# Optimization experiments

Hardware: AMD Instinct MI355X
Metric: run time of the kernel (lower is better)

## Reference

```python
import jax, jax.numpy as jnp
import numpy as np

E = 128            # emb_size
N_TEXT = 40000     # text entities
N_NONTEXT = 10000  # non-text entities
N = N_TEXT + N_NONTEXT
N_EDGES = 300000
N_REL = 500
I = 3              # num_intents
ROUNDS = 2
RROUNDS = 2
PE = 2             # topic one-hot width
PRED_IN = 5 * E + 2 * PE + 2 * PE * (ROUNDS + RROUNDS)  # 5*128+4+16 = 660


def setup_inputs() -> dict:
    key = jax.random.key(0)
    ks = jax.random.split(key, 12)
    return {
        "h_id_tensor": jax.random.randint(ks[0], (N_EDGES,), 0, N, dtype=jnp.int64 if jax.config.jax_enable_x64 else jnp.int32).astype(jnp.int32),
        "r_id_tensor": jax.random.randint(ks[1], (N_EDGES,), 0, N_REL).astype(jnp.int32),
        "t_id_tensor": jax.random.randint(ks[2], (N_EDGES,), 0, N).astype(jnp.int32),
        "q_emb": jax.random.normal(ks[3], (1, E), dtype=jnp.float32),
        "entity_embs": jax.random.normal(ks[4], (N_TEXT, E), dtype=jnp.float32),
        "num_non_text_entities": N_NONTEXT,
        "relation_embs": jax.random.normal(ks[5], (N_REL, E), dtype=jnp.float32),
        "topic_entity_one_hot": jax.random.uniform(ks[6], (N, PE), dtype=jnp.float32),
        # learned params
        "non_text_entity_emb": jax.random.normal(ks[7], (1, E), dtype=jnp.float32),
        "intent_embs": jax.random.normal(ks[8], (I, E), dtype=jnp.float32),
        "W1": jax.random.normal(ks[9], (PRED_IN, E), dtype=jnp.float32) * 0.02,
        "b1": jnp.zeros((E,), dtype=jnp.float32),
        "W2": jax.random.normal(ks[10], (E, 1), dtype=jnp.float32) * 0.02,
        "b2": jnp.zeros((1,), dtype=jnp.float32),
    }


def _peconv(x, src, dst, n, inv_cnt):
    # mean aggregation: gather x at src, scatter-mean into dst
    s = jax.ops.segment_sum(x[src], dst, num_segments=n)
    return s * inv_cnt


def reference(h_id_tensor, r_id_tensor, t_id_tensor, q_emb, entity_embs,
              num_non_text_entities, relation_embs, topic_entity_one_hot,
              non_text_entity_emb, intent_embs, W1, b1, W2, b2):
    n = topic_entity_one_hot.shape[0]
    h_e0 = jnp.concatenate(
        [entity_embs, jnp.broadcast_to(non_text_entity_emb, (num_non_text_entities, E))], axis=0)  # [N,E]

    ones = jnp.ones((h_id_tensor.shape[0], 1), jnp.float32)
    cnt_fwd = jax.ops.segment_sum(ones, t_id_tensor, num_segments=n)  # in-degree via (h->t)
    cnt_rev = jax.ops.segment_sum(ones, h_id_tensor, num_segments=n)
    inv_fwd = 1.0 / jnp.maximum(cnt_fwd, 1.0)
    inv_rev = 1.0 / jnp.maximum(cnt_rev, 1.0)

    h_e_list = [h_e0, topic_entity_one_hot]
    h_pe = topic_entity_one_hot
    for _ in range(ROUNDS):
        h_pe = _peconv(h_pe, h_id_tensor, t_id_tensor, n, inv_fwd)
        h_e_list.append(h_pe)
    h_pe = topic_entity_one_hot
    for _ in range(RROUNDS):
        h_pe = _peconv(h_pe, t_id_tensor, h_id_tensor, n, inv_rev)
        h_e_list.append(h_pe)
    h_e = jnp.concatenate(h_e_list, axis=1)  # [N, E + 2 + 2*4]

    h_r = relation_embs[r_id_tensor]         # [T, E]
    h_head = h_e[h_id_tensor]                # [T, E+10]
    h_tail = h_e[t_id_tensor]                # [T, E+10]
    T = h_r.shape[0]
    h_q = jnp.broadcast_to(q_emb, (T, E))

    logits = []
    for i in range(intent_embs.shape[0]):
        iv = jnp.broadcast_to(intent_embs[i][None, :], (T, E))
        h_triple = jnp.concatenate([iv, h_q, h_head, h_r, h_tail], axis=1)  # [T, PRED_IN]
        h = jnp.maximum(h_triple @ W1 + b1, 0.0)
        logits.append(h @ W2 + b2)
    return jnp.concatenate(logits, axis=1)  # [T, I]
```

## Files before the change

### kernel.cpp

```cpp
#include <hip/hip_runtime.h>

#define E 128
#define OFF_Q 128
#define OFF_HEAD 256
#define OFF_REL 394
#define OFF_TAIL 522
#define KTOT 138
#define KP 160
#define AST 168
#define RNGC 2048
#define NCHK 8
#define CAP 16384

typedef __attribute__((ext_vector_type(8))) short short8;
typedef __attribute__((ext_vector_type(4))) float f32x4;

__device__ __forceinline__ unsigned short f2bf(float f) {
    unsigned u = __float_as_uint(f);
    return (unsigned short)((u + 0x7fffu + ((u >> 16) & 1u)) >> 16);
}
__device__ __forceinline__ unsigned bpack(float lo, float hi) {
    return (unsigned)f2bf(lo) | ((unsigned)f2bf(hi) << 16);
}
__device__ __forceinline__ float blo(unsigned u) { return __uint_as_float(u << 16); }
__device__ __forceinline__ float bhi(unsigned u) { return __uint_as_float(u & 0xffff0000u); }

__global__ __launch_bounds__(256) void bucket_prep_kernel(
        const int* __restrict__ h_id, const int* __restrict__ t_id,
        const float* __restrict__ rel, const float* __restrict__ intent,
        const float* __restrict__ q, const float* __restrict__ W1,
        const float* __restrict__ b1,
        unsigned* __restrict__ curs, unsigned* __restrict__ pairs_f,
        unsigned* __restrict__ pairs_r,
        unsigned short* __restrict__ rel_bf, float* __restrict__ bias3,
        unsigned short* __restrict__ W1T,
        int T, int bucketBlocks, int relBlocks, int biasBlocks, int NREL) {
    int tid = threadIdx.x;
    int bid = blockIdx.x;

    if (bid < bucketBlocks) {
        __shared__ unsigned hf[32], hr[32], basef[32], baser[32];
        if (tid < 32) { hf[tid] = 0; hr[tid] = 0; }
        __syncthreads();
        int e0 = (bid * 256 + tid) * 4;
        int hh[4], tt[4];
        int cnt = 0;
        if (e0 < T) {
            if (e0 + 3 < T) {
                int4 h4 = *(const int4*)&h_id[e0];
                int4 t4 = *(const int4*)&t_id[e0];
                hh[0] = h4.x; hh[1] = h4.y; hh[2] = h4.z; hh[3] = h4.w;
                tt[0] = t4.x; tt[1] = t4.y; tt[2] = t4.z; tt[3] = t4.w;
                cnt = 4;
            } else {
                for (int j = 0; e0 + j < T && j < 4; ++j) {
                    hh[j] = h_id[e0 + j];
                    tt[j] = t_id[e0 + j];
                    ++cnt;
                }
            }
        }
        unsigned bf[4], br[4];
        for (int j = 0; j < cnt; ++j) {
            bf[j] = (unsigned)tt[j] >> 11;
            br[j] = (unsigned)hh[j] >> 11;
            atomicAdd(&hf[bf[j]], 1u);
            atomicAdd(&hr[br[j]], 1u);
        }
        __syncthreads();
        if (tid < 32) {
            basef[tid] = hf[tid] ? atomicAdd(&curs[tid], hf[tid]) : 0u;
            baser[tid] = hr[tid] ? atomicAdd(&curs[32 + tid], hr[tid]) : 0u;
        }
        __syncthreads();
        if (tid < 32) { hf[tid] = 0; hr[tid] = 0; }
        __syncthreads();
        for (int j = 0; j < cnt; ++j) {
            unsigned sf = basef[bf[j]] + atomicAdd(&hf[bf[j]], 1u);
            if (sf < CAP) pairs_f[bf[j] * CAP + sf] =
                (unsigned)hh[j] | (((unsigned)tt[j] & 2047u) << 16);
            unsigned sr = baser[br[j]] + atomicAdd(&hr[br[j]], 1u);
            if (sr < CAP) pairs_r[br[j] * CAP + sr] =
                (unsigned)tt[j] | (((unsigned)hh[j] & 2047u) << 16);
        }
    } else if (bid < bucketBlocks + relBlocks) {
        int idx = (bid - bucketBlocks) * 256 + tid;
        int r = idx >> 7, j = idx & 127;
        if (r < NREL) {
            const float4* xr = (const float4*)(rel + (size_t)r * E);
            float acc = 0.f;
#pragma unroll
            for (int k4 = 0; k4 < 32; ++k4) {
                float4 x = xr[k4];
                int k = OFF_REL + k4 * 4;
                acc = fmaf(x.x, W1[(k + 0) * E + j], acc);
                acc = fmaf(x.y, W1[(k + 1) * E + j], acc);
                acc = fmaf(x.z, W1[(k + 2) * E + j], acc);
                acc = fmaf(x.w, W1[(k + 3) * E + j], acc);
            }
            rel_bf[idx] = f2bf(acc);
        }
    } else if (bid < bucketBlocks + relBlocks + biasBlocks) {
        int widx = (bid - bucketBlocks - relBlocks) * 4 + (tid >> 6);
        int lane = tid & 63;
        if (widx < 384) {
            int i = widx >> 7, j = widx & 127;
            float sum = 0.f;
#pragma unroll
            for (int m = 0; m < 4; ++m) {
                int k = lane + 64 * m;
                float x = (k < 128) ? intent[i * E + k] : q[k - 128];
                sum = fmaf(x, W1[(size_t)k * E + j], sum);
            }
#pragma unroll
            for (int o = 32; o > 0; o >>= 1) sum += __shfl_xor(sum, o, 64);
            if (lane == 0) bias3[i * E + j] = sum + b1[j];
        }
    } else {
        int c = bid - bucketBlocks - relBlocks - biasBlocks;
        if (tid < KP) {
            int cc = (c < 128) ? c : c - 128;
            int base = (c < 128) ? OFF_HEAD : OFF_TAIL;
            float v = (tid < KTOT) ? W1[(size_t)(base + tid) * E + cc] : 0.f;
            W1T[(size_t)c * KP + tid] = f2bf(v);
        }
    }
}

__global__ __launch_bounds__(1024) void scat1_kernel(
        const unsigned* __restrict__ pairs_f, const unsigned* __restrict__ pairs_r,
        const unsigned* __restrict__ curs, const float* __restrict__ topic,
        float* __restrict__ part1) {
    __shared__ float bins[6][RNGC];
    int b = blockIdx.x;
    int ck = blockIdx.y;
    int tid = threadIdx.x;
    for (int i = tid; i < 6 * RNGC; i += 1024) ((float*)bins)[i] = 0.f;
    __syncthreads();
    unsigned cf = min(curs[b], (unsigned)CAP);
    unsigned cr = min(curs[32 + b], (unsigned)CAP);
    const unsigned* pf = pairs_f + (size_t)b * CAP;
    const unsigned* pr = pairs_r + (size_t)b * CAP;
    unsigned lf = (cf + NCHK - 1) / NCHK;
    unsigned lr = (cr + NCHK - 1) / NCHK;
    unsigned f0 = ck * lf, f1e = min(cf, f0 + lf);
    unsigned r0 = ck * lr, r1e = min(cr, r0 + lr);
    for (unsigned i = f0 + tid; i < f1e; i += 1024) {
        unsigned p = pf[i];
        float2 v = *(const float2*)&topic[2 * (size_t)(p & 0xFFFFu)];
        int dl = p >> 16;
        atomicAdd(&bins[0][dl], v.x);
        atomicAdd(&bins[1][dl], v.y);
        atomicAdd(&bins[2][dl], 1.0f);
    }
    for (unsigned i = r0 + tid; i < r1e; i += 1024) {
        unsigned p = pr[i];
        float2 v = *(const float2*)&topic[2 * (size_t)(p & 0xFFFFu)];
        int dl = p >> 16;
        atomicAdd(&bins[3][dl], v.x);
        atomicAdd(&bins[4][dl], v.y);
        atomicAdd(&bins[5][dl], 1.0f);
    }
    __syncthreads();
    float* dst = part1 + ((size_t)(b * NCHK + ck) * 6) * RNGC;
#pragma unroll
    for (int c = 0; c < 6; ++c)
        for (int n = tid; n < RNGC; n += 1024)
            dst[c * RNGC + n] = bins[c][n];
}

__global__ __launch_bounds__(256) void reduce1_kernel(
        const float* __restrict__ part1,
        float* __restrict__ pef1, float* __restrict__ per1,
        float* __restrict__ inv_fwd, float* __restrict__ inv_rev, int N) {
    int n = blockIdx.x * 256 + threadIdx.x;
    if (n >= N) return;
    int b = n >> 11, nl = n & 2047;
    float s[6] = {0.f, 0.f, 0.f, 0.f, 0.f, 0.f};
    const float* base = part1 + (size_t)b * NCHK * 6 * RNGC + nl;
#pragma unroll
    for (int ck = 0; ck < NCHK; ++ck)
#pragma unroll
        for (int c = 0; c < 6; ++c)
            s[c] += base[(ck * 6 + c) * RNGC];
    float invf = 1.0f / fmaxf(s[2], 1.0f);
    float invr = 1.0f / fmaxf(s[5], 1.0f);
    pef1[2 * n] = s[0] * invf;
    pef1[2 * n + 1] = s[1] * invf;
    per1[2 * n] = s[3] * invr;
    per1[2 * n + 1] = s[4] * invr;
    inv_fwd[n] = invf;
    inv_rev[n] = invr;
}

__global__ __launch_bounds__(1024) void scat2_kernel(
        const unsigned* __restrict__ pairs_f, const unsigned* __restrict__ pairs_r,
        const unsigned* __restrict__ curs,
        const float* __restrict__ pef1, const float* __restrict__ per1,
        float* __restrict__ part2) {
    __shared__ float bins[4][RNGC];
    int b = blockIdx.x;
    int ck = blockIdx.y;
    int tid = threadIdx.x;
    for (int i = tid; i < 4 * RNGC; i += 1024) ((float*)bins)[i] = 0.f;
    __syncthreads();
    unsigned cf = min(curs[b], (unsigned)CAP);
    unsigned cr = min(curs[32 + b], (unsigned)CAP);
    const unsigned* pf = pairs_f + (size_t)b * CAP;
    const unsigned* pr = pairs_r + (size_t)b * CAP;
    unsigned lf = (cf + NCHK - 1) / NCHK;
    unsigned lr = (cr + NCHK - 1) / NCHK;
    unsigned f0 = ck * lf, f1e = min(cf, f0 + lf);
    unsigned r0 = ck * lr, r1e = min(cr, r0 + lr);
    for (unsigned i = f0 + tid; i < f1e; i += 1024) {
        unsigned p = pf[i];
        float2 v = *(const float2*)&pef1[2 * (size_t)(p & 0xFFFFu)];
        int dl = p >> 16;
        atomicAdd(&bins[0][dl], v.x);
        atomicAdd(&bins[1][dl], v.y);
    }
    for (unsigned i = r0 + tid; i < r1e; i += 1024) {
        unsigned p = pr[i];
        float2 v = *(const float2*)&per1[2 * (size_t)(p & 0xFFFFu)];
        int dl = p >> 16;
        atomicAdd(&bins[2][dl], v.x);
        atomicAdd(&bins[3][dl], v.y);
    }
    __syncthreads();
    float* dst = part2 + ((size_t)(b * NCHK + ck) * 4) * RNGC;
#pragma unroll
    for (int c = 0; c < 4; ++c)
        for (int n = tid; n < RNGC; n += 1024)
            dst[c * RNGC + n] = bins[c][n];
}

__global__ __launch_bounds__(256) void nodepre_mfma(
        const float* __restrict__ ent, const float* __restrict__ nontext,
        const float* __restrict__ topic,
        const float* __restrict__ pef1, const float* __restrict__ per1,
        const float* __restrict__ part2,
        const float* __restrict__ inv_fwd, const float* __restrict__ inv_rev,
        const unsigned short* __restrict__ W1T,
        unsigned short* __restrict__ head_bf, unsigned short* __restrict__ tail_bf,
        int N, int NTEXT) {
    __shared__ unsigned short As[64 * AST];
    int t = threadIdx.x;
    int lane = t & 63;
    int w = t >> 6;
    int l15 = lane & 15;
    int lg = lane >> 4;
    int n0 = blockIdx.x * 64;

    {
        int row = t >> 2, ch = t & 3;
        int node = n0 + row;
        bool ok = node < N;
        const float* src = (node < NTEXT) ? (ent + (size_t)node * E) : nontext;
        unsigned* dst = (unsigned*)&As[row * AST + ch * 32];
#pragma unroll
        for (int qq = 0; qq < 8; ++qq) {
            float4 v = ok ? *(const float4*)(src + ch * 32 + qq * 4)
                          : make_float4(0.f, 0.f, 0.f, 0.f);
            dst[qq * 2 + 0] = bpack(v.x, v.y);
            dst[qq * 2 + 1] = bpack(v.z, v.w);
        }
    }
    if (t < 64) {
        int node = n0 + t;
        bool ok = node < N;
        unsigned short* dst = &As[t * AST + 128];
        float ex[6];
        if (ok) {
            ex[0] = topic[2 * (size_t)node]; ex[1] = topic[2 * (size_t)node + 1];
            ex[2] = pef1[2 * (size_t)node];  ex[3] = pef1[2 * (size_t)node + 1];
            ex[4] = per1[2 * (size_t)node];  ex[5] = per1[2 * (size_t)node + 1];
        } else {
#pragma unroll
            for (int m = 0; m < 6; ++m) ex[m] = 0.f;
        }
        dst[0] = f2bf(ex[0]); dst[1] = f2bf(ex[1]);
        dst[2] = f2bf(ex[2]); dst[3] = f2bf(ex[3]);
        dst[6] = f2bf(ex[4]); dst[7] = f2bf(ex[5]);
#pragma unroll
        for (int m = 10; m < 32; ++m) dst[m] = 0;
    }
    {
        int nloc = t >> 2;
        int c = t & 3;
        int node = n0 + nloc;
        float val = 0.f;
        if (node < N) {
            int b = node >> 11, nl = node & 2047;
            const float* base = part2 + (size_t)b * NCHK * 4 * RNGC + nl;
            float s = 0.f;
#pragma unroll
            for (int ck = 0; ck < NCHK; ++ck)
                s += base[(ck * 4 + c) * RNGC];
            val = s * ((c < 2) ? inv_fwd[node] : inv_rev[node]);
        }
        int slot = (c < 2) ? (132 + c) : (134 + c);
        As[nloc * AST + (slot - 128) + 128] = f2bf(val);
    }
    __syncthreads();

    f32x4 zero = {0.f, 0.f, 0.f, 0.f};
    f32x4 acc[4][4];
#pragma unroll
    for (int rt = 0; rt < 4; ++rt)
#pragma unroll
        for (int ct = 0; ct < 4; ++ct) acc[rt][ct] = zero;

#pragma unroll
    for (int ks = 0; ks < 5; ++ks) {
        int kb = ks * 32 + lg * 8;
        short8 afrag[4];
#pragma unroll
        for (int rt = 0; rt < 4; ++rt)
            afrag[rt] = *(const short8*)&As[(rt * 16 + l15) * AST + kb];
#pragma unroll
        for (int ct = 0; ct < 4; ++ct) {
            int c = w * 64 + ct * 16 + l15;
            short8 b = *(const short8*)&W1T[(size_t)c * KP + kb];
#pragma unroll
            for (int rt = 0; rt < 4; ++rt)
                acc[rt][ct] = __builtin_amdgcn_mfma_f32_16x16x32_bf16(
                    afrag[rt], b, acc[rt][ct], 0, 0, 0);
        }
    }

#pragma unroll
    for (int rt = 0; rt < 4; ++rt) {
#pragma unroll
        for (int ct = 0; ct < 4; ++ct) {
            int c = w * 64 + ct * 16 + l15;
            unsigned short* base = (c < 128) ? head_bf : tail_bf;
            int cc = (c < 128) ? c : c - 128;
#pragma unroll
            for (int r = 0; r < 4; ++r) {
                int node = n0 + rt * 16 + lg * 4 + r;
                if (node < N) base[(size_t)node * E + cc] = f2bf(acc[rt][ct][r]);
            }
        }
    }
}

__global__ __launch_bounds__(256) void edge_kernel(
        const int* __restrict__ h_id, const int* __restrict__ r_id, const int* __restrict__ t_id,
        const unsigned short* __restrict__ head_bf, const unsigned short* __restrict__ rel_bf,
        const unsigned short* __restrict__ tail_bf, const float* __restrict__ bias3,
        const float* __restrict__ W2, const float* __restrict__ b2,
        float* __restrict__ out, int T) {
    int lane = threadIdx.x & 63;
    int sub = lane >> 4;
    int sl = lane & 15;
    int wid = blockIdx.x * (blockDim.x >> 6) + (threadIdx.x >> 6);
    int nw = gridDim.x * (blockDim.x >> 6);
    int c0 = sl * 8;

    float4 bi0a = *(const float4*)&bias3[c0],         bi0b = *(const float4*)&bias3[c0 + 4];
    float4 bi1a = *(const float4*)&bias3[E + c0],     bi1b = *(const float4*)&bias3[E + c0 + 4];
    float4 bi2a = *(const float4*)&bias3[2 * E + c0], bi2b = *(const float4*)&bias3[2 * E + c0 + 4];
    float4 w2a = *(const float4*)&W2[c0], w2b = *(const float4*)&W2[c0 + 4];
    float b2s = b2[0];

    int qd = lane / 3;
    int md = lane - qd * 3;

    int ne4 = (T + 3) >> 2;
    for (int e4 = wid; e4 < ne4; e4 += nw) {
        int e = e4 * 4 + sub;
        float p0 = 0.f, p1 = 0.f, p2 = 0.f;
        if (e < T) {
            int h = h_id[e], r = r_id[e], tt = t_id[e];
            uint4 hu = *(const uint4*)(head_bf + (size_t)h * E + c0);
            uint4 ru = *(const uint4*)(rel_bf + (size_t)r * E + c0);
            uint4 tu = *(const uint4*)(tail_bf + (size_t)tt * E + c0);
            float sv[8];
            sv[0] = blo(hu.x) + blo(ru.x) + blo(tu.x);
            sv[1] = bhi(hu.x) + bhi(ru.x) + bhi(tu.x);
            sv[2] = blo(hu.y) + blo(ru.y) + blo(tu.y);
            sv[3] = bhi(hu.y) + bhi(ru.y) + bhi(tu.y);
            sv[4] = blo(hu.z) + blo(ru.z) + blo(tu.z);
            sv[5] = bhi(hu.z) + bhi(ru.z) + bhi(tu.z);
            sv[6] = blo(hu.w) + blo(ru.w) + blo(tu.w);
            sv[7] = bhi(hu.w) + bhi(ru.w) + bhi(tu.w);
            float bi0[8] = {bi0a.x, bi0a.y, bi0a.z, bi0a.w, bi0b.x, bi0b.y, bi0b.z, bi0b.w};
            float bi1[8] = {bi1a.x, bi1a.y, bi1a.z, bi1a.w, bi1b.x, bi1b.y, bi1b.z, bi1b.w};
            float bi2[8] = {bi2a.x, bi2a.y, bi2a.z, bi2a.w, bi2b.x, bi2b.y, bi2b.z, bi2b.w};
            float w2v[8] = {w2a.x, w2a.y, w2a.z, w2a.w, w2b.x, w2b.y, w2b.z, w2b.w};
#pragma unroll
            for (int j = 0; j < 8; ++j) {
                p0 = fmaf(fmaxf(sv[j] + bi0[j], 0.f), w2v[j], p0);
                p1 = fmaf(fmaxf(sv[j] + bi1[j], 0.f), w2v[j], p1);
                p2 = fmaf(fmaxf(sv[j] + bi2[j], 0.f), w2v[j], p2);
            }
        }
#pragma unroll
        for (int o = 1; o < 16; o <<= 1) {
            p0 += __shfl_xor(p0, o, 64);
            p1 += __shfl_xor(p1, o, 64);
            p2 += __shfl_xor(p2, o, 64);
        }
        if (e4 * 4 + 3 < T) {
            int srcl = qd * 16;
            float v0 = __shfl(p0, srcl, 64);
            float v1 = __shfl(p1, srcl, 64);
            float v2 = __shfl(p2, srcl, 64);
            if (lane < 12) {
                float v = (md == 0) ? v0 : ((md == 1) ? v1 : v2);
                out[(size_t)e4 * 12 + lane] = v + b2s;
            }
        } else if (e < T && sl < 3) {
            float v = (sl == 0) ? p0 : ((sl == 1) ? p1 : p2);
            out[(size_t)e * 3 + sl] = v + b2s;
        }
    }
}

extern "C" void kernel_launch(void* const* d_in, const int* in_sizes, int n_in,
                              void* d_out, int out_size, void* d_ws, size_t ws_size,
                              hipStream_t stream) {
    const int* h_id = (const int*)d_in[0];
    const int* r_id = (const int*)d_in[1];
    const int* t_id = (const int*)d_in[2];
    const float* q = (const float*)d_in[3];
    const float* ent = (const float*)d_in[4];
    const float* rel = (const float*)d_in[6];
    const float* topic = (const float*)d_in[7];
    const float* nontext = (const float*)d_in[8];
    const float* intent = (const float*)d_in[9];
    const float* W1 = (const float*)d_in[10];
    const float* b1 = (const float*)d_in[11];
    const float* W2 = (const float*)d_in[12];
    const float* b2 = (const float*)d_in[13];

    int T = in_sizes[0];
    int NTEXT = in_sizes[4] / E;
    int N = in_sizes[7] / 2;
    int NREL = in_sizes[6] / E;

    int RC = (N + RNGC - 1) / RNGC;

    unsigned* curs = (unsigned*)d_ws;
    unsigned* pairs_f = curs + 64;
    unsigned* pairs_r = pairs_f + (size_t)32 * CAP;
    float* part1 = (float*)(pairs_r + (size_t)32 * CAP);
    float* inv_fwd = part1 + (size_t)RC * NCHK * 6 * RNGC;
    float* inv_rev = inv_fwd + N;
    float* pef1 = inv_rev + N;
    float* per1 = pef1 + 2 * (size_t)N;
    float* bias3 = per1 + 2 * (size_t)N;
    unsigned short* W1T = (unsigned short*)(bias3 + 3 * E);
    unsigned short* rel_bf = W1T + 256 * KP;
    unsigned short* head_bf = rel_bf + (size_t)NREL * E;
    unsigned short* tail_bf = head_bf + (size_t)N * E;

    const int tb = 256;
    int bucketBlocks = (T + tb * 4 - 1) / (tb * 4);
    int relBlocks = (NREL * E + tb - 1) / tb;
    int biasBlocks = 96;

    hipMemsetAsync(curs, 0, 64 * sizeof(unsigned), stream);

    bucket_prep_kernel<<<bucketBlocks + relBlocks + biasBlocks + 256, tb, 0, stream>>>(
        h_id, t_id, rel, intent, q, W1, b1, curs, pairs_f, pairs_r,
        rel_bf, bias3, W1T, T, bucketBlocks, relBlocks, biasBlocks, NREL);
    scat1_kernel<<<dim3(RC, NCHK), 1024, 0, stream>>>(pairs_f, pairs_r, curs, topic, part1);
    reduce1_kernel<<<(N + tb - 1) / tb, tb, 0, stream>>>(part1, pef1, per1, inv_fwd, inv_rev, N);
    scat2_kernel<<<dim3(RC, NCHK), 1024, 0, stream>>>(pairs_f, pairs_r, curs, pef1, per1, part1);
    nodepre_mfma<<<(N + 63) / 64, tb, 0, stream>>>(ent, nontext, topic, pef1, per1,
                                                   part1, inv_fwd, inv_rev, W1T,
                                                   head_bf, tail_bf, N, NTEXT);
    edge_kernel<<<2048, tb, 0, stream>>>(h_id, r_id, t_id, head_bf, rel_bf, tail_bf,
                                         bias3, W2, b2, (float*)d_out, T);
}
```

Baseline: 111.2 us.

## Fuse bucketing and scatter phases into one cooperative kernel with grid syncs

Merges edge bucketing, first scatter, reduction and second scatter into a single cooperative kernel separated by grid.sync, replacing four launches plus a memset. Weight preprocessing moves into its own kernel. The aim is to cut launch overhead and inter-kernel gaps. The grid is only RC*NCHK = 200 blocks of 1024 threads each holding 48KB of LDS, so bucketing runs with fewer threads and the cooperative launch requires all blocks to be co-resident. The edge kernel also drops its vectorized 12-lane output store in favour of the simpler per-edge store.

```diff
diff --git a/kernel.cpp b/kernel.cpp
--- a/kernel.cpp
+++ b/kernel.cpp
@@ -1,4 +1,7 @@
 #include <hip/hip_runtime.h>
+#include <hip/hip_cooperative_groups.h>
+
+namespace cg = cooperative_groups;
 
 #define E 128
 #define OFF_Q 128
@@ -25,24 +28,26 @@
 __device__ __forceinline__ float blo(unsigned u) { return __uint_as_float(u << 16); }
 __device__ __forceinline__ float bhi(unsigned u) { return __uint_as_float(u & 0xffff0000u); }
 
-__global__ __launch_bounds__(256) void bucket_prep_kernel(
+__global__ __launch_bounds__(1024) void scatter_coop(
         const int* __restrict__ h_id, const int* __restrict__ t_id,
-        const float* __restrict__ rel, const float* __restrict__ intent,
-        const float* __restrict__ q, const float* __restrict__ W1,
-        const float* __restrict__ b1,
+        const float* __restrict__ topic,
         unsigned* __restrict__ curs, unsigned* __restrict__ pairs_f,
-        unsigned* __restrict__ pairs_r,
-        unsigned short* __restrict__ rel_bf, float* __restrict__ bias3,
-        unsigned short* __restrict__ W1T,
-        int T, int bucketBlocks, int relBlocks, int biasBlocks, int NREL) {
+        unsigned* __restrict__ pairs_r, float* __restrict__ part1,
+        float* __restrict__ pef1, float* __restrict__ per1,
+        float* __restrict__ inv_fwd, float* __restrict__ inv_rev,
+        int T, int N) {
+    cg::grid_group grid = cg::this_grid();
+    __shared__ float bins[6][RNGC];
+    __shared__ unsigned hf[32], hr[32], basef[32], baser[32];
     int tid = threadIdx.x;
     int bid = blockIdx.x;
-
-    if (bid < bucketBlocks) {
-        __shared__ unsigned hf[32], hr[32], basef[32], baser[32];
-        if (tid < 32) { hf[tid] = 0; hr[tid] = 0; }
-        __syncthreads();
-        int e0 = (bid * 256 + tid) * 4;
+    int gthreads = gridDim.x * 1024;
+
+    if (bid == 0 && tid < 64) curs[tid] = 0;
+    grid.sync();
+
+    for (int base = 0; base < T; base += gthreads * 4) {
+        int e0 = base + (bid * 1024 + tid) * 4;
         int hh[4], tt[4];
         int cnt = 0;
         if (e0 < T) {
@@ -60,6 +65,8 @@
                 }
             }
         }
+        if (tid < 32) { hf[tid] = 0; hr[tid] = 0; }
+        __syncthreads();
         unsigned bf[4], br[4];
         for (int j = 0; j < cnt; ++j) {
             bf[j] = (unsigned)tt[j] >> 11;
@@ -83,8 +90,115 @@
             if (sr < CAP) pairs_r[br[j] * CAP + sr] =
                 (unsigned)tt[j] | (((unsigned)hh[j] & 2047u) << 16);
         }
-    } else if (bid < bucketBlocks + relBlocks) {
-        int idx = (bid - bucketBlocks) * 256 + tid;
+        __syncthreads();
+    }
+    grid.sync();
+
+    {
+        int b = bid / NCHK;
+        int ck = bid % NCHK;
+        for (int i = tid; i < 6 * RNGC; i += 1024) ((float*)bins)[i] = 0.f;
+        __syncthreads();
+        unsigned cf = min(curs[b], (unsigned)CAP);
+        unsigned cr = min(curs[32 + b], (unsigned)CAP);
+        const unsigned* pf = pairs_f + (size_t)b * CAP;
+        const unsigned* pr = pairs_r + (size_t)b * CAP;
+        unsigned lf = (cf + NCHK - 1) / NCHK;
+        unsigned lr = (cr + NCHK - 1) / NCHK;
+        unsigned f0 = ck * lf, f1e = min(cf, f0 + lf);
+        unsigned r0 = ck * lr, r1e = min(cr, r0 + lr);
+        for (unsigned i = f0 + tid; i < f1e; i += 1024) {
+            unsigned p = pf[i];
+            float2 v = *(const float2*)&topic[2 * (size_t)(p & 0xFFFFu)];
+            int dl = p >> 16;
+            atomicAdd(&bins[0][dl], v.x);
+            atomicAdd(&bins[1][dl], v.y);
+            atomicAdd(&bins[2][dl], 1.0f);
+        }
+        for (unsigned i = r0 + tid; i < r1e; i += 1024) {
+            unsigned p = pr[i];
+            float2 v = *(const float2*)&topic[2 * (size_t)(p & 0xFFFFu)];
+            int dl = p >> 16;
+            atomicAdd(&bins[3][dl], v.x);
+            atomicAdd(&bins[4][dl], v.y);
+            atomicAdd(&bins[5][dl], 1.0f);
+        }
+        __syncthreads();
+        float* dst = part1 + ((size_t)(b * NCHK + ck) * 6) * RNGC;
+#pragma unroll
+        for (int c = 0; c < 6; ++c)
+            for (int n = tid; n < RNGC; n += 1024)
+                dst[c * RNGC + n] = bins[c][n];
+    }
+    grid.sync();
+
+    for (int n = bid * 1024 + tid; n < N; n += gthreads) {
+        int b = n >> 11, nl = n & 2047;
+        float s[6] = {0.f, 0.f, 0.f, 0.f, 0.f, 0.f};
+        const float* pbase = part1 + (size_t)b * NCHK * 6 * RNGC + nl;
+#pragma unroll
+        for (int ck = 0; ck < NCHK; ++ck)
+#pragma unroll
+            for (int c = 0; c < 6; ++c)
+                s[c] += pbase[(ck * 6 + c) * RNGC];
+        float invf = 1.0f / fmaxf(s[2], 1.0f);
+        float invr = 1.0f / fmaxf(s[5], 1.0f);
+        pef1[2 * n] = s[0] * invf;
+        pef1[2 * n + 1] = s[1] * invf;
+        per1[2 * n] = s[3] * invr;
+        per1[2 * n + 1] = s[4] * invr;
+        inv_fwd[n] = invf;
+        inv_rev[n] = invr;
+    }
+    grid.sync();
+
+    {
+        int b = bid / NCHK;
+        int ck = bid % NCHK;
+        for (int i = tid; i < 4 * RNGC; i += 1024) ((float*)bins)[i] = 0.f;
+        __syncthreads();
+        unsigned cf = min(curs[b], (unsigned)CAP);
+        unsigned cr = min(curs[32 + b], (unsigned)CAP);
+        const unsigned* pf = pairs_f + (size_t)b * CAP;
+        const unsigned* pr = pairs_r + (size_t)b * CAP;
+        unsigned lf = (cf + NCHK - 1) / NCHK;
+        unsigned lr = (cr + NCHK - 1) / NCHK;
+        unsigned f0 = ck * lf, f1e = min(cf, f0 + lf);
+        unsigned r0 = ck * lr, r1e = min(cr, r0 + lr);
+        for (unsigned i = f0 + tid; i < f1e; i += 1024) {
+            unsigned p = pf[i];
+            float2 v = *(const float2*)&pef1[2 * (size_t)(p & 0xFFFFu)];
+            int dl = p >> 16;
+            atomicAdd(&bins[0][dl], v.x);
+            atomicAdd(&bins[1][dl], v.y);
+        }
+        for (unsigned i = r0 + tid; i < r1e; i += 1024) {
+            unsigned p = pr[i];
+            float2 v = *(const float2*)&per1[2 * (size_t)(p & 0xFFFFu)];
+            int dl = p >> 16;
+            atomicAdd(&bins[2][dl], v.x);
+            atomicAdd(&bins[3][dl], v.y);
+        }
+        __syncthreads();
+        float* dst = part1 + ((size_t)(b * NCHK + ck) * 4) * RNGC;
+#pragma unroll
+        for (int c = 0; c < 4; ++c)
+            for (int n = tid; n < RNGC; n += 1024)
+                dst[c * RNGC + n] = bins[c][n];
+    }
+}
+
+__global__ __launch_bounds__(256) void prep_kernel(
+        const float* __restrict__ rel, const float* __restrict__ intent,
+        const float* __restrict__ q, const float* __restrict__ W1,
+        const float* __restrict__ b1,
+        unsigned short* __restrict__ rel_bf, float* __restrict__ bias3,
+        unsigned short* __restrict__ W1T,
+        int relBlocks, int biasBlocks, int NREL) {
+    int tid = threadIdx.x;
+    int bid = blockIdx.x;
+    if (bid < relBlocks) {
+        int idx = bid * 256 + tid;
         int r = idx >> 7, j = idx & 127;
         if (r < NREL) {
             const float4* xr = (const float4*)(rel + (size_t)r * E);
@@ -100,8 +214,8 @@
             }
             rel_bf[idx] = f2bf(acc);
         }
-    } else if (bid < bucketBlocks + relBlocks + biasBlocks) {
-        int widx = (bid - bucketBlocks - relBlocks) * 4 + (tid >> 6);
+    } else if (bid < relBlocks + biasBlocks) {
+        int widx = (bid - relBlocks) * 4 + (tid >> 6);
         int lane = tid & 63;
         if (widx < 384) {
             int i = widx >> 7, j = widx & 127;
@@ -117,7 +231,7 @@
             if (lane == 0) bias3[i * E + j] = sum + b1[j];
         }
     } else {
-        int c = bid - bucketBlocks - relBlocks - biasBlocks;
+        int c = bid - relBlocks - biasBlocks;
         if (tid < KP) {
             int cc = (c < 128) ? c : c - 128;
             int base = (c < 128) ? OFF_HEAD : OFF_TAIL;
@@ -125,113 +239,6 @@
             W1T[(size_t)c * KP + tid] = f2bf(v);
         }
     }
-}
-
-__global__ __launch_bounds__(1024) void scat1_kernel(
-        const unsigned* __restrict__ pairs_f, const unsigned* __restrict__ pairs_r,
-        const unsigned* __restrict__ curs, const float* __restrict__ topic,
-        float* __restrict__ part1) {
-    __shared__ float bins[6][RNGC];
-    int b = blockIdx.x;
-    int ck = blockIdx.y;
-    int tid = threadIdx.x;
-    for (int i = tid; i < 6 * RNGC; i += 1024) ((float*)bins)[i] = 0.f;
-    __syncthreads();
-    unsigned cf = min(curs[b], (unsigned)CAP);
-    unsigned cr = min(curs[32 + b], (unsigned)CAP);
-    const unsigned* pf = pairs_f + (size_t)b * CAP;
-    const unsigned* pr = pairs_r + (size_t)b * CAP;
-    unsigned lf = (cf + NCHK - 1) / NCHK;
-    unsigned lr = (cr + NCHK - 1) / NCHK;
-    unsigned f0 = ck * lf, f1e = min(cf, f0 + lf);
-    unsigned r0 = ck * lr, r1e = min(cr, r0 + lr);
-    for (unsigned i = f0 + tid; i < f1e; i += 1024) {
-        unsigned p = pf[i];
-        float2 v = *(const float2*)&topic[2 * (size_t)(p & 0xFFFFu)];
-        int dl = p >> 16;
-        atomicAdd(&bins[0][dl], v.x);
-        atomicAdd(&bins[1][dl], v.y);
-        atomicAdd(&bins[2][dl], 1.0f);
-    }
-    for (unsigned i = r0 + tid; i < r1e; i += 1024) {
-        unsigned p = pr[i];
-        float2 v = *(const float2*)&topic[2 * (size_t)(p & 0xFFFFu)];
-        int dl = p >> 16;
-        atomicAdd(&bins[3][dl], v.x);
-        atomicAdd(&bins[4][dl], v.y);
-        atomicAdd(&bins[5][dl], 1.0f);
-    }
-    __syncthreads();
-    float* dst = part1 + ((size_t)(b * NCHK + ck) * 6) * RNGC;
-#pragma unroll
-    for (int c = 0; c < 6; ++c)
-        for (int n = tid; n < RNGC; n += 1024)
-            dst[c * RNGC + n] = bins[c][n];
-}
-
-__global__ __launch_bounds__(256) void reduce1_kernel(
-        const float* __restrict__ part1,
-        float* __restrict__ pef1, float* __restrict__ per1,
-        float* __restrict__ inv_fwd, float* __restrict__ inv_rev, int N) {
-    int n = blockIdx.x * 256 + threadIdx.x;
-    if (n >= N) return;
-    int b = n >> 11, nl = n & 2047;
-    float s[6] = {0.f, 0.f, 0.f, 0.f, 0.f, 0.f};
-    const float* base = part1 + (size_t)b * NCHK * 6 * RNGC + nl;
-#pragma unroll
-    for (int ck = 0; ck < NCHK; ++ck)
-#pragma unroll
-        for (int c = 0; c < 6; ++c)
-            s[c] += base[(ck * 6 + c) * RNGC];
-    float invf = 1.0f / fmaxf(s[2], 1.0f);
-    float invr = 1.0f / fmaxf(s[5], 1.0f);
-    pef1[2 * n] = s[0] * invf;
-    pef1[2 * n + 1] = s[1] * invf;
-    per1[2 * n] = s[3] * invr;
-    per1[2 * n + 1] = s[4] * invr;
-    inv_fwd[n] = invf;
-    inv_rev[n] = invr;
-}
-
-__global__ __launch_bounds__(1024) void scat2_kernel(
-        const unsigned* __restrict__ pairs_f, const unsigned* __restrict__ pairs_r,
-        const unsigned* __restrict__ curs,
-        const float* __restrict__ pef1, const float* __restrict__ per1,
-        float* __restrict__ part2) {
-    __shared__ float bins[4][RNGC];
-    int b = blockIdx.x;
-    int ck = blockIdx.y;
-    int tid = threadIdx.x;
-    for (int i = tid; i < 4 * RNGC; i += 1024) ((float*)bins)[i] = 0.f;
-    __syncthreads();
-    unsigned cf = min(curs[b], (unsigned)CAP);
-    unsigned cr = min(curs[32 + b], (unsigned)CAP);
-    const unsigned* pf = pairs_f + (size_t)b * CAP;
-    const unsigned* pr = pairs_r + (size_t)b * CAP;
-    unsigned lf = (cf + NCHK - 1) / NCHK;
-    unsigned lr = (cr + NCHK - 1) / NCHK;
-    unsigned f0 = ck * lf, f1e = min(cf, f0 + lf);
-    unsigned r0 = ck * lr, r1e = min(cr, r0 + lr);
-    for (unsigned i = f0 + tid; i < f1e; i += 1024) {
-        unsigned p = pf[i];
-        float2 v = *(const float2*)&pef1[2 * (size_t)(p & 0xFFFFu)];
-        int dl = p >> 16;
-        atomicAdd(&bins[0][dl], v.x);
-        atomicAdd(&bins[1][dl], v.y);
-    }
-    for (unsigned i = r0 + tid; i < r1e; i += 1024) {
-        unsigned p = pr[i];
-        float2 v = *(const float2*)&per1[2 * (size_t)(p & 0xFFFFu)];
-        int dl = p >> 16;
-        atomicAdd(&bins[2][dl], v.x);
-        atomicAdd(&bins[3][dl], v.y);
-    }
-    __syncthreads();
-    float* dst = part2 + ((size_t)(b * NCHK + ck) * 4) * RNGC;
-#pragma unroll
-    for (int c = 0; c < 4; ++c)
-        for (int n = tid; n < RNGC; n += 1024)
-            dst[c * RNGC + n] = bins[c][n];
 }
 
 __global__ __launch_bounds__(256) void nodepre_mfma(
@@ -362,9 +369,6 @@
     float4 bi2a = *(const float4*)&bias3[2 * E + c0], bi2b = *(const float4*)&bias3[2 * E + c0 + 4];
     float4 w2a = *(const float4*)&W2[c0], w2b = *(const float4*)&W2[c0 + 4];
     float b2s = b2[0];
-
-    int qd = lane / 3;
-    int md = lane - qd * 3;
 
     int ne4 = (T + 3) >> 2;
     for (int e4 = wid; e4 < ne4; e4 += nw) {
@@ -401,16 +405,7 @@
             p1 += __shfl_xor(p1, o, 64);
             p2 += __shfl_xor(p2, o, 64);
         }
-        if (e4 * 4 + 3 < T) {
-            int srcl = qd * 16;
-            float v0 = __shfl(p0, srcl, 64);
-            float v1 = __shfl(p1, srcl, 64);
-            float v2 = __shfl(p2, srcl, 64);
-            if (lane < 12) {
-                float v = (md == 0) ? v0 : ((md == 1) ? v1 : v2);
-                out[(size_t)e4 * 12 + lane] = v + b2s;
-            }
-        } else if (e < T && sl < 3) {
+        if (e < T && sl < 3) {
             float v = (sl == 0) ? p0 : ((sl == 1) ? p1 : p2);
             out[(size_t)e * 3 + sl] = v + b2s;
         }
@@ -456,18 +451,23 @@
     unsigned short* tail_bf = head_bf + (size_t)N * E;
 
     const int tb = 256;
-    int bucketBlocks = (T + tb * 4 - 1) / (tb * 4);
     int relBlocks = (NREL * E + tb - 1) / tb;
     int biasBlocks = 96;
 
-    hipMemsetAsync(curs, 0, 64 * sizeof(unsigned), stream);
-
-    bucket_prep_kernel<<<bucketBlocks + relBlocks + biasBlocks + 256, tb, 0, stream>>>(
-        h_id, t_id, rel, intent, q, W1, b1, curs, pairs_f, pairs_r,
-        rel_bf, bias3, W1T, T, bucketBlocks, relBlocks, biasBlocks, NREL);
-    scat1_kernel<<<dim3(RC, NCHK), 1024, 0, stream>>>(pairs_f, pairs_r, curs, topic, part1);
-    reduce1_kernel<<<(N + tb - 1) / tb, tb, 0, stream>>>(part1, pef1, per1, inv_fwd, inv_rev, N);
-    scat2_kernel<<<dim3(RC, NCHK), 1024, 0, stream>>>(pairs_f, pairs_r, curs, pef1, per1, part1);
+    prep_kernel<<<relBlocks + biasBlocks + 256, tb, 0, stream>>>(
+        rel, intent, q, W1, b1, rel_bf, bias3, W1T, relBlocks, biasBlocks, NREL);
+
+    {
+        int Tl = T, Nl = N;
+        void* args[] = {(void*)&h_id, (void*)&t_id, (void*)&topic,
+                        (void*)&curs, (void*)&pairs_f, (void*)&pairs_r,
+                        (void*)&part1, (void*)&pef1, (void*)&per1,
+                        (void*)&inv_fwd, (void*)&inv_rev,
+                        (void*)&Tl, (void*)&Nl};
+        hipLaunchCooperativeKernel((void*)scatter_coop, dim3(RC * NCHK), dim3(1024),
+                                   args, 0, stream);
+    }
+
     nodepre_mfma<<<(N + 63) / 64, tb, 0, stream>>>(ent, nontext, topic, pef1, per1,
                                                    part1, inv_fwd, inv_rev, W1T,
                                                    head_bf, tail_bf, N, NTEXT);
```

After: 200.4 us. 80.3% more time.
